# Kernel optimization log

Hardware: AMD Instinct MI355X
Metric: run time of the kernel (lower is better)

The kernel has to match this reference:

```python
import jax, jax.numpy as jnp
import numpy as np
import math

B, S, D, H = 2, 2048, 1024, 16
DH = D // H


def setup_inputs() -> dict:
    key = jax.random.key(0)
    ks = jax.random.split(key, 10)
    scale = 1.0 / math.sqrt(D)
    inp = {
        "x": jax.random.normal(ks[0], (B, S, D), dtype=jnp.float32),
        "valid_nums": jax.random.randint(ks[1], (B,), 1, S + 1, dtype=jnp.int32),
        "Wq": jax.random.normal(ks[2], (D, D), dtype=jnp.float32) * scale,
        "bq": jnp.zeros((D,), dtype=jnp.float32),
        "Wk": jax.random.normal(ks[3], (D, D), dtype=jnp.float32) * scale,
        "bk": jnp.zeros((D,), dtype=jnp.float32),
        "Wv": jax.random.normal(ks[4], (D, D), dtype=jnp.float32) * scale,
        "bv": jnp.zeros((D,), dtype=jnp.float32),
        "Wo": jax.random.normal(ks[5], (D, D), dtype=jnp.float32) * scale,
        "bo": jnp.zeros((D,), dtype=jnp.float32),
    }
    return inp


def _split_heads(t):
    # (B, S, D) -> (B, H, S, DH)
    return t.reshape(B, S, H, DH).transpose(0, 2, 1, 3)


def reference(x, valid_nums, Wq, bq, Wk, bk, Wv, bv, Wo, bo):
    q = _split_heads(x @ Wq + bq)
    k = _split_heads(x @ Wk + bk)
    v = _split_heads(x @ Wv + bv)
    scores = jnp.einsum("bhqd,bhkd->bhqk", q, k) / math.sqrt(DH)  # (B,H,S,S)
    # length mask over keys: key j valid iff j < valid_nums[b]
    key_mask = jnp.arange(S)[None, :] < valid_nums[:, None]        # (B,S)
    scores = jnp.where(key_mask[:, None, None, :], scores, -jnp.inf)
    attn = jax.nn.softmax(scores, axis=-1)
    out = jnp.einsum("bhqk,bhkd->bhqd", attn, v)                   # (B,H,S,DH)
    out = out.transpose(0, 2, 1, 3).reshape(B, S, D)
    return out @ Wo + bo
```

## Files before the change

kernel.cpp:

```cpp
#include <hip/hip_runtime.h>
#include <hip/hip_bf16.h>
#include <math.h>

static constexpr int Bb = 2, Ss = 2048, Dd = 1024, Hh = 16, DHh = 64;
static constexpr int Mm = Bb * Ss;
static constexpr int Kk = Dd;

typedef __attribute__((ext_vector_type(8))) short bf16x8;
typedef __attribute__((ext_vector_type(4))) float f32x4;
typedef unsigned short us;

__device__ inline short f2b(float f) {
    __hip_bfloat16 h = __float2bfloat16(f);
    return *reinterpret_cast<short*>(&h);
}
__device__ inline float b2f(us u) {
    __hip_bfloat16 h = *reinterpret_cast<__hip_bfloat16*>(&u);
    return __bfloat162float(h);
}
__device__ inline unsigned pk2(float lo, float hi) {
    return ((unsigned)(us)f2b(hi) << 16) | (unsigned)(us)f2b(lo);
}

__device__ inline void gload16(us* lds, const us* g) {
    __builtin_amdgcn_global_load_lds(
        (const __attribute__((address_space(1))) void*)g,
        (__attribute__((address_space(3))) void*)lds,
        16, 0, 0);
}

__global__ __launch_bounds__(256)
void xconv_kernel(const float* __restrict__ x, us* __restrict__ xb)
{
    const size_t i = ((size_t)blockIdx.x * 256 + threadIdx.x) * 8;
    float4 a = *(const float4*)(x + i);
    float4 b = *(const float4*)(x + i + 4);
    bf16x8 t;
    t[0] = f2b(a.x); t[1] = f2b(a.y); t[2] = f2b(a.z); t[3] = f2b(a.w);
    t[4] = f2b(b.x); t[5] = f2b(b.y); t[6] = f2b(b.z); t[7] = f2b(b.w);
    *(bf16x8*)(xb + i) = t;
}

__global__ __launch_bounds__(256)
void wtrans_kernel(const float* __restrict__ W, us* __restrict__ Wth,
                   us* __restrict__ Wtl, int split)
{
    __shared__ float T[64][65];
    const int n0 = blockIdx.x * 64, k0 = blockIdx.y * 64;
    const int tid = threadIdx.x;
    const int r = tid >> 2, c0 = (tid & 3) * 16;
#pragma unroll
    for (int j = 0; j < 4; ++j) {
        float4 v = *(const float4*)(W + (size_t)(k0 + r) * Dd + n0 + c0 + 4 * j);
        T[r][c0 + 4 * j + 0] = v.x;
        T[r][c0 + 4 * j + 1] = v.y;
        T[r][c0 + 4 * j + 2] = v.z;
        T[r][c0 + 4 * j + 3] = v.w;
    }
    __syncthreads();
    us hi[16], lo[16];
#pragma unroll
    for (int j = 0; j < 16; ++j) {
        float v = T[c0 + j][r];
        us h = (us)f2b(v);
        hi[j] = h;
        if (split) lo[j] = (us)f2b(v - b2f(h));
    }
    *(bf16x8*)&Wth[(size_t)(n0 + r) * Kk + k0 + c0]     = *(bf16x8*)&hi[0];
    *(bf16x8*)&Wth[(size_t)(n0 + r) * Kk + k0 + c0 + 8] = *(bf16x8*)&hi[8];
    if (split) {
        *(bf16x8*)&Wtl[(size_t)(n0 + r) * Kk + k0 + c0]     = *(bf16x8*)&lo[0];
        *(bf16x8*)&Wtl[(size_t)(n0 + r) * Kk + k0 + c0 + 8] = *(bf16x8*)&lo[8];
    }
}

__global__ __launch_bounds__(256)
void gemm_qkv_kernel(const us* __restrict__ xb, const us* __restrict__ Wt,
                     const float* __restrict__ bq, const float* __restrict__ bk,
                     const float* __restrict__ bv, us* __restrict__ QKV)
{
    __shared__ us As[128 * 64];
    __shared__ us Bs[128 * 64];
    const int tid = threadIdx.x;
    const int wave = tid >> 6, lane = tid & 63;
    const int wr = wave >> 1, wc = wave & 1;
    const int lg = lane >> 4, ll = lane & 15;
    const int col0 = blockIdx.x * 128;
    const int row0 = blockIdx.y * 128;

    f32x4 acc[4][4];
#pragma unroll
    for (int mt = 0; mt < 4; ++mt)
#pragma unroll
        for (int nt = 0; nt < 4; ++nt)
#pragma unroll
            for (int r = 0; r < 4; ++r) acc[mt][nt][r] = 0.f;

    const us* Ag = xb + (size_t)(row0 + wave * 32 + (lane >> 3)) * Kk + (lane & 7) * 8;
    const us* Bg = Wt + (size_t)(col0 + wave * 32 + (lane >> 3)) * Kk + (lane & 7) * 8;
    us* Ad = &As[(wave * 4) * 512];
    us* Bd = &Bs[(wave * 4) * 512];

    for (int k0 = 0; k0 < Kk; k0 += 64) {
        __syncthreads();
#pragma unroll
        for (int i = 0; i < 4; ++i) {
            gload16(Ad + i * 512, Ag + (size_t)(i * 8) * Kk + k0);
            gload16(Bd + i * 512, Bg + (size_t)(i * 8) * Kk + k0);
        }
        __syncthreads();
#pragma unroll
        for (int ks = 0; ks < 2; ++ks) {
            bf16x8 af[4], bfr[4];
#pragma unroll
            for (int mt = 0; mt < 4; ++mt)
                af[mt] = *(const bf16x8*)&As[(wr * 64 + mt * 16 + ll) * 64 + ks * 32 + lg * 8];
#pragma unroll
            for (int nt = 0; nt < 4; ++nt)
                bfr[nt] = *(const bf16x8*)&Bs[(wc * 64 + nt * 16 + ll) * 64 + ks * 32 + lg * 8];
#pragma unroll
            for (int mt = 0; mt < 4; ++mt)
#pragma unroll
                for (int nt = 0; nt < 4; ++nt)
                    acc[mt][nt] = __builtin_amdgcn_mfma_f32_16x16x32_bf16(af[mt], bfr[nt], acc[mt][nt], 0, 0, 0);
        }
    }

    const int z = col0 >> 10;
    const int c0 = col0 & 1023;
    const float* bias = (z == 0) ? bq : (z == 1) ? bk : bv;
    us* outz = QKV + (size_t)z * Mm * Dd;

    if (z == 2) {
#pragma unroll
        for (int mt = 0; mt < 4; ++mt)
#pragma unroll
            for (int nt = 0; nt < 4; ++nt) {
                int row = row0 + wr * 64 + mt * 16 + lg * 4;
                int col = c0 + wc * 64 + nt * 16 + ll;
                int b_ = row >> 11, s_ = row & 2047;
                float bv_ = bias[col];
                union { us u[4]; uint2 d2; } pk;
#pragma unroll
                for (int r = 0; r < 4; ++r) pk.u[r] = (us)f2b(acc[mt][nt][r] + bv_);
                *(uint2*)&outz[((size_t)(b_ * Hh * DHh) + col) * Ss + s_] = pk.d2;
            }
    } else {
#pragma unroll
        for (int mt = 0; mt < 4; ++mt)
#pragma unroll
            for (int nt = 0; nt < 4; ++nt)
#pragma unroll
                for (int r = 0; r < 4; ++r) {
                    int row = row0 + wr * 64 + mt * 16 + lg * 4 + r;
                    int col = c0 + wc * 64 + nt * 16 + ll;
                    float v = acc[mt][nt][r] + bias[col];
                    int b_ = row >> 11, s_ = row & 2047, h_ = col >> 6, d_ = col & 63;
                    outz[(((size_t)(b_ * Hh + h_)) * Ss + s_) * DHh + d_] = (us)f2b(v);
                }
    }
}

__global__ __launch_bounds__(256)
void gemm_final_kernel(const us* __restrict__ Oh, const us* __restrict__ Ol,
                       const us* __restrict__ Wth, const us* __restrict__ Wtl,
                       const float* __restrict__ bo, float* __restrict__ out)
{
    __shared__ us AhS[128 * 64];
    __shared__ us AlS[128 * 64];
    __shared__ us BhS[64 * 64];
    __shared__ us BlS[64 * 64];
    const int tid = threadIdx.x;
    const int wave = tid >> 6, lane = tid & 63;
    const int wr = wave >> 1, wc = wave & 1;
    const int lg = lane >> 4, ll = lane & 15;
    const int col0 = blockIdx.x * 64;
    const int row0 = blockIdx.y * 128;

    f32x4 acc[4][2];
#pragma unroll
    for (int mt = 0; mt < 4; ++mt)
#pragma unroll
        for (int nt = 0; nt < 2; ++nt)
#pragma unroll
            for (int r = 0; r < 4; ++r) acc[mt][nt][r] = 0.f;

    const size_t aoff = (size_t)(row0 + wave * 32 + (lane >> 3)) * Kk + (lane & 7) * 8;
    const size_t boff = (size_t)(col0 + wave * 16 + (lane >> 3)) * Kk + (lane & 7) * 8;
    const us* Ahg = Oh + aoff;
    const us* Alg = Ol + aoff;
    const us* Bhg = Wth + boff;
    const us* Blg = Wtl + boff;
    us* AhD = &AhS[(wave * 4) * 512];
    us* AlD = &AlS[(wave * 4) * 512];
    us* BhD = &BhS[(wave * 2) * 512];
    us* BlD = &BlS[(wave * 2) * 512];

    for (int k0 = 0; k0 < Kk; k0 += 64) {
        __syncthreads();
#pragma unroll
        for (int i = 0; i < 4; ++i) {
            gload16(AhD + i * 512, Ahg + (size_t)(i * 8) * Kk + k0);
            gload16(AlD + i * 512, Alg + (size_t)(i * 8) * Kk + k0);
        }
#pragma unroll
        for (int j = 0; j < 2; ++j) {
            gload16(BhD + j * 512, Bhg + (size_t)(j * 8) * Kk + k0);
            gload16(BlD + j * 512, Blg + (size_t)(j * 8) * Kk + k0);
        }
        __syncthreads();
#pragma unroll
        for (int ks = 0; ks < 2; ++ks) {
            bf16x8 ah[4], al[4], bh[2], bl[2];
#pragma unroll
            for (int mt = 0; mt < 4; ++mt) {
                ah[mt] = *(const bf16x8*)&AhS[(wr * 64 + mt * 16 + ll) * 64 + ks * 32 + lg * 8];
                al[mt] = *(const bf16x8*)&AlS[(wr * 64 + mt * 16 + ll) * 64 + ks * 32 + lg * 8];
            }
#pragma unroll
            for (int nt = 0; nt < 2; ++nt) {
                bh[nt] = *(const bf16x8*)&BhS[(wc * 32 + nt * 16 + ll) * 64 + ks * 32 + lg * 8];
                bl[nt] = *(const bf16x8*)&BlS[(wc * 32 + nt * 16 + ll) * 64 + ks * 32 + lg * 8];
            }
#pragma unroll
            for (int mt = 0; mt < 4; ++mt)
#pragma unroll
                for (int nt = 0; nt < 2; ++nt) {
                    acc[mt][nt] = __builtin_amdgcn_mfma_f32_16x16x32_bf16(ah[mt], bh[nt], acc[mt][nt], 0, 0, 0);
                    acc[mt][nt] = __builtin_amdgcn_mfma_f32_16x16x32_bf16(al[mt], bh[nt], acc[mt][nt], 0, 0, 0);
                    acc[mt][nt] = __builtin_amdgcn_mfma_f32_16x16x32_bf16(ah[mt], bl[nt], acc[mt][nt], 0, 0, 0);
                }
        }
    }

#pragma unroll
    for (int mt = 0; mt < 4; ++mt)
#pragma unroll
        for (int nt = 0; nt < 2; ++nt)
#pragma unroll
            for (int r = 0; r < 4; ++r) {
                int row = row0 + wr * 64 + mt * 16 + lg * 4 + r;
                int col = col0 + wc * 32 + nt * 16 + ll;
                out[(size_t)row * Dd + col] = acc[mt][nt][r] + bo[col];
            }
}

__global__ __launch_bounds__(256)
void attn_mfma_kernel(const us* __restrict__ Q, const us* __restrict__ K,
                      const us* __restrict__ Vt_g, const int* __restrict__ valid_nums,
                      us* __restrict__ Oh, us* __restrict__ Ol)
{
    const int bh = blockIdx.y;
    const int b  = bh >> 4, h = bh & 15;
    const int q0 = blockIdx.x * 64;
    const int tid  = threadIdx.x;
    const int wave = tid >> 6;
    const int lane = tid & 63;
    const int lg = lane >> 4;
    const int ll = lane & 15;

    const int nv = valid_nums[b];
    const int ntiles = (nv + 63) >> 6;

    const us* Qb = Q    + (size_t)bh * Ss * DHh;
    const us* Kb = K    + (size_t)bh * Ss * DHh;
    const us* Vb = Vt_g + (size_t)bh * DHh * Ss;

    __shared__ us Ks[64][68];
    __shared__ us Vs[64][68];

    bf16x8 qa[2];
    {
        const us* qrow = Qb + (size_t)(q0 + wave * 16 + ll) * DHh;
        qa[0] = *(const bf16x8*)(qrow + lg * 8);
        qa[1] = *(const bf16x8*)(qrow + 32 + lg * 8);
    }

    f32x4 o[4];
#pragma unroll
    for (int nt = 0; nt < 4; ++nt) { o[nt][0]=0.f; o[nt][1]=0.f; o[nt][2]=0.f; o[nt][3]=0.f; }
    float mq = -INFINITY, lq = 0.f;

    const int srow = tid >> 2;
    const int scol = (tid & 3) * 16;
    const float sc = 0.125f;

    for (int kt = 0; kt < ntiles; ++kt) {
        const int k0 = kt * 64;
        __syncthreads();
        {
            const us* Kr = Kb + (size_t)(k0 + srow) * DHh + scol;
            *(bf16x8*)&Ks[srow][scol]     = *(const bf16x8*)Kr;
            *(bf16x8*)&Ks[srow][scol + 8] = *(const bf16x8*)(Kr + 8);
            const us* Vr = Vb + (size_t)srow * Ss + k0 + scol;
            *(bf16x8*)&Vs[srow][scol]     = *(const bf16x8*)Vr;
            *(bf16x8*)&Vs[srow][scol + 8] = *(const bf16x8*)(Vr + 8);
        }
        __syncthreads();

        f32x4 s[4];
#pragma unroll
        for (int nt = 0; nt < 4; ++nt) { s[nt][0]=0.f; s[nt][1]=0.f; s[nt][2]=0.f; s[nt][3]=0.f; }
#pragma unroll
        for (int ks = 0; ks < 2; ++ks) {
#pragma unroll
            for (int nt = 0; nt < 4; ++nt) {
                bf16x8 kf = *(const bf16x8*)&Ks[nt * 16 + ll][ks * 32 + lg * 8];
                s[nt] = __builtin_amdgcn_mfma_f32_16x16x32_bf16(kf, qa[ks], s[nt], 0, 0, 0);
            }
        }

        float p[4][4];
        float mx = -INFINITY;
#pragma unroll
        for (int nt = 0; nt < 4; ++nt)
#pragma unroll
            for (int r = 0; r < 4; ++r) {
                int key = k0 + nt * 16 + lg * 4 + r;
                float v = (key < nv) ? s[nt][r] * sc : -INFINITY;
                p[nt][r] = v;
                mx = fmaxf(mx, v);
            }
        mx = fmaxf(mx, __shfl_xor(mx, 16));
        mx = fmaxf(mx, __shfl_xor(mx, 32));
        float mn = fmaxf(mq, mx);
        float corr = __expf(mq - mn);
        mq = mn;
        float ps = 0.f;
#pragma unroll
        for (int nt = 0; nt < 4; ++nt)
#pragma unroll
            for (int r = 0; r < 4; ++r) {
                float pv = __expf(p[nt][r] - mn);
                p[nt][r] = pv;
                ps += pv;
            }
        ps += __shfl_xor(ps, 16);
        ps += __shfl_xor(ps, 32);
        lq = lq * corr + ps;

        unsigned dw[4][2];
#pragma unroll
        for (int nt = 0; nt < 4; ++nt) {
            dw[nt][0] = pk2(p[nt][0], p[nt][1]);
            dw[nt][1] = pk2(p[nt][2], p[nt][3]);
        }

        float corr4[4];
#pragma unroll
        for (int r = 0; r < 4; ++r) corr4[r] = __shfl(corr, lg * 16 + lg * 4 + r);
#pragma unroll
        for (int nt = 0; nt < 4; ++nt)
#pragma unroll
            for (int r = 0; r < 4; ++r) o[nt][r] *= corr4[r];

        const int sA = ((2 * lg) & 3) * 16 + ll;
        const int sB = ((2 * lg + 1) & 3) * 16 + ll;
        const bool hi = (lg & 2);
#pragma unroll
        for (int ks = 0; ks < 2; ++ks) {
            unsigned a0 = (unsigned)__shfl((int)dw[2 * ks][0],     sA);
            unsigned a1 = (unsigned)__shfl((int)dw[2 * ks][1],     sA);
            unsigned a2 = (unsigned)__shfl((int)dw[2 * ks][0],     sB);
            unsigned a3 = (unsigned)__shfl((int)dw[2 * ks][1],     sB);
            unsigned b0 = (unsigned)__shfl((int)dw[2 * ks + 1][0], sA);
            unsigned b1 = (unsigned)__shfl((int)dw[2 * ks + 1][1], sA);
            unsigned b2 = (unsigned)__shfl((int)dw[2 * ks + 1][0], sB);
            unsigned b3 = (unsigned)__shfl((int)dw[2 * ks + 1][1], sB);
            union { unsigned w[4]; bf16x8 v; } pa;
            pa.w[0] = hi ? b0 : a0;
            pa.w[1] = hi ? b1 : a1;
            pa.w[2] = hi ? b2 : a2;
            pa.w[3] = hi ? b3 : a3;
#pragma unroll
            for (int nt = 0; nt < 4; ++nt) {
                bf16x8 vb = *(const bf16x8*)&Vs[nt * 16 + ll][ks * 32 + lg * 8];
                o[nt] = __builtin_amdgcn_mfma_f32_16x16x32_bf16(pa.v, vb, o[nt], 0, 0, 0);
            }
        }
    }

    float linv[4];
#pragma unroll
    for (int r = 0; r < 4; ++r) linv[r] = 1.f / __shfl(lq, lg * 16 + lg * 4 + r);
#pragma unroll
    for (int r = 0; r < 4; ++r) {
        int row = q0 + wave * 16 + lg * 4 + r;
#pragma unroll
        for (int nt = 0; nt < 4; ++nt) {
            float val = o[nt][r] * linv[r];
            us uh = (us)f2b(val);
            float rem = val - b2f(uh);
            size_t base = ((size_t)b * Ss + row) * Dd + h * DHh + nt * 16 + ll;
            Oh[base] = uh;
            Ol[base] = (us)f2b(rem);
        }
    }
}

extern "C" void kernel_launch(void* const* d_in, const int* in_sizes, int n_in,
                              void* d_out, int out_size, void* d_ws, size_t ws_size,
                              hipStream_t stream) {
    const float* x     = (const float*)d_in[0];
    const int*   valid = (const int*)d_in[1];
    const float* Wq = (const float*)d_in[2];
    const float* bq = (const float*)d_in[3];
    const float* Wk = (const float*)d_in[4];
    const float* bk = (const float*)d_in[5];
    const float* Wv = (const float*)d_in[6];
    const float* bv = (const float*)d_in[7];
    const float* Wo = (const float*)d_in[8];
    const float* bo = (const float*)d_in[9];

    const size_t per = (size_t)Mm * Dd;
    const size_t wsz = (size_t)Dd * Kk;
    us* wsp  = (us*)d_ws;
    us* QKV  = wsp;
    us* Wt   = QKV + 3 * per;
    us* OhB  = Wt + 3 * wsz;
    us* OlB  = OhB + per;
    us* Woth = OlB + per;
    us* Wotl = Woth + wsz;
    us* xb   = Wotl + wsz;

    xconv_kernel<<<(Mm * Kk) / (256 * 8), 256, 0, stream>>>(x, xb);

    dim3 tg(Dd / 64, Kk / 64);
    wtrans_kernel<<<tg, 256, 0, stream>>>(Wq, Wt + 0 * wsz, nullptr, 0);
    wtrans_kernel<<<tg, 256, 0, stream>>>(Wk, Wt + 1 * wsz, nullptr, 0);
    wtrans_kernel<<<tg, 256, 0, stream>>>(Wv, Wt + 2 * wsz, nullptr, 0);
    wtrans_kernel<<<tg, 256, 0, stream>>>(Wo, Woth, Wotl, 1);

    gemm_qkv_kernel<<<dim3(3 * Dd / 128, Mm / 128), 256, 0, stream>>>(
        xb, Wt, bq, bk, bv, QKV);

    attn_mfma_kernel<<<dim3(Ss / 64, Bb * Hh), 256, 0, stream>>>(
        QKV, QKV + per, QKV + 2 * per, valid, OhB, OlB);

    gemm_final_kernel<<<dim3(Dd / 64, Mm / 128), 256, 0, stream>>>(
        OhB, OlB, Woth, Wotl, bo, (float*)d_out);
}
```

Baseline: 166.1 us.

## Fold softmax scale into Q, lazy rescale, MFMA row sums, merge weight transposes

Folds the 1/sqrt(DH) scale into the Q projection epilogue and skips key masking on full tiles. The online-softmax rescale now runs only when some row max grows by more than a threshold. Row sums come from an extra MFMA against a ones vector instead of shuffle reductions, so probabilities are summed after bf16 rounding. The four weight-transpose launches become one 3D-grid launch, which removes launch overhead at the cost of some per-block branching.

Measured after the change: 155.1 us. -6.6%, faster.

```diff
diff --git a/kernel.cpp b/kernel.cpp
--- a/kernel.cpp
+++ b/kernel.cpp
@@ -42,10 +42,17 @@
 }
 
 __global__ __launch_bounds__(256)
-void wtrans_kernel(const float* __restrict__ W, us* __restrict__ Wth,
-                   us* __restrict__ Wtl, int split)
+void wtrans_kernel(const float* __restrict__ Wq, const float* __restrict__ Wk,
+                   const float* __restrict__ Wv, const float* __restrict__ Wo,
+                   us* __restrict__ Wt, us* __restrict__ Woth, us* __restrict__ Wotl)
 {
     __shared__ float T[64][65];
+    const int z = blockIdx.z;
+    const float* W = (z == 0) ? Wq : (z == 1) ? Wk : (z == 2) ? Wv : Wo;
+    const int split = (z == 3);
+    us* dh = split ? Woth : (Wt + (size_t)z * Dd * Kk);
+    us* dl = Wotl;
+
     const int n0 = blockIdx.x * 64, k0 = blockIdx.y * 64;
     const int tid = threadIdx.x;
     const int r = tid >> 2, c0 = (tid & 3) * 16;
@@ -66,11 +73,11 @@
         hi[j] = h;
         if (split) lo[j] = (us)f2b(v - b2f(h));
     }
-    *(bf16x8*)&Wth[(size_t)(n0 + r) * Kk + k0 + c0]     = *(bf16x8*)&hi[0];
-    *(bf16x8*)&Wth[(size_t)(n0 + r) * Kk + k0 + c0 + 8] = *(bf16x8*)&hi[8];
+    *(bf16x8*)&dh[(size_t)(n0 + r) * Kk + k0 + c0]     = *(bf16x8*)&hi[0];
+    *(bf16x8*)&dh[(size_t)(n0 + r) * Kk + k0 + c0 + 8] = *(bf16x8*)&hi[8];
     if (split) {
-        *(bf16x8*)&Wtl[(size_t)(n0 + r) * Kk + k0 + c0]     = *(bf16x8*)&lo[0];
-        *(bf16x8*)&Wtl[(size_t)(n0 + r) * Kk + k0 + c0 + 8] = *(bf16x8*)&lo[8];
+        *(bf16x8*)&dl[(size_t)(n0 + r) * Kk + k0 + c0]     = *(bf16x8*)&lo[0];
+        *(bf16x8*)&dl[(size_t)(n0 + r) * Kk + k0 + c0 + 8] = *(bf16x8*)&lo[8];
     }
 }
 
@@ -129,6 +136,7 @@
     const int z = col0 >> 10;
     const int c0 = col0 & 1023;
     const float* bias = (z == 0) ? bq : (z == 1) ? bk : bv;
+    const float osc = (z == 0) ? 0.125f : 1.0f;
     us* outz = QKV + (size_t)z * Mm * Dd;
 
     if (z == 2) {
@@ -154,7 +162,7 @@
                 for (int r = 0; r < 4; ++r) {
                     int row = row0 + wr * 64 + mt * 16 + lg * 4 + r;
                     int col = c0 + wc * 64 + nt * 16 + ll;
-                    float v = acc[mt][nt][r] + bias[col];
+                    float v = (acc[mt][nt][r] + bias[col]) * osc;
                     int b_ = row >> 11, s_ = row & 2047, h_ = col >> 6, d_ = col & 63;
                     outz[(((size_t)(b_ * Hh + h_)) * Ss + s_) * DHh + d_] = (us)f2b(v);
                 }
@@ -276,14 +284,19 @@
         qa[1] = *(const bf16x8*)(qrow + 32 + lg * 8);
     }
 
-    f32x4 o[4];
+    union { unsigned w[4]; bf16x8 v; } ones_u;
+#pragma unroll
+    for (int i = 0; i < 4; ++i) ones_u.w[i] = 0x3F803F80u;
+    const bf16x8 vones = ones_u.v;
+
+    f32x4 o[4], o4;
 #pragma unroll
     for (int nt = 0; nt < 4; ++nt) { o[nt][0]=0.f; o[nt][1]=0.f; o[nt][2]=0.f; o[nt][3]=0.f; }
-    float mq = -INFINITY, lq = 0.f;
+    o4[0]=0.f; o4[1]=0.f; o4[2]=0.f; o4[3]=0.f;
+    float mq = -INFINITY;
 
     const int srow = tid >> 2;
     const int scol = (tid & 3) * 16;
-    const float sc = 0.125f;
 
     for (int kt = 0; kt < ntiles; ++kt) {
         const int k0 = kt * 64;
@@ -311,33 +324,52 @@
         }
 
         float p[4][4];
-        float mx = -INFINITY;
-#pragma unroll
-        for (int nt = 0; nt < 4; ++nt)
-#pragma unroll
-            for (int r = 0; r < 4; ++r) {
-                int key = k0 + nt * 16 + lg * 4 + r;
-                float v = (key < nv) ? s[nt][r] * sc : -INFINITY;
-                p[nt][r] = v;
-                mx = fmaxf(mx, v);
-            }
+        float mx;
+        if (k0 + 64 <= nv) {
+#pragma unroll
+            for (int nt = 0; nt < 4; ++nt)
+#pragma unroll
+                for (int r = 0; r < 4; ++r) p[nt][r] = s[nt][r];
+            mx = fmaxf(fmaxf(fmaxf(p[0][0], p[0][1]), fmaxf(p[0][2], p[0][3])),
+                       fmaxf(fmaxf(p[1][0], p[1][1]), fmaxf(p[1][2], p[1][3])));
+            mx = fmaxf(mx,
+                 fmaxf(fmaxf(fmaxf(p[2][0], p[2][1]), fmaxf(p[2][2], p[2][3])),
+                       fmaxf(fmaxf(p[3][0], p[3][1]), fmaxf(p[3][2], p[3][3]))));
+        } else {
+            mx = -INFINITY;
+#pragma unroll
+            for (int nt = 0; nt < 4; ++nt)
+#pragma unroll
+                for (int r = 0; r < 4; ++r) {
+                    int key = k0 + nt * 16 + lg * 4 + r;
+                    float v = (key < nv) ? s[nt][r] : -INFINITY;
+                    p[nt][r] = v;
+                    mx = fmaxf(mx, v);
+                }
+        }
         mx = fmaxf(mx, __shfl_xor(mx, 16));
         mx = fmaxf(mx, __shfl_xor(mx, 32));
-        float mn = fmaxf(mq, mx);
-        float corr = __expf(mq - mn);
-        mq = mn;
-        float ps = 0.f;
+
+        const bool rescale = !__all(mx <= mq + 8.f);
+        if (rescale) {
+            float mn = fmaxf(mq, mx);
+            float corr = __expf(mq - mn);
+            mq = mn;
+            float corr4[4];
+#pragma unroll
+            for (int r = 0; r < 4; ++r) corr4[r] = __shfl(corr, lg * 16 + lg * 4 + r);
+#pragma unroll
+            for (int nt = 0; nt < 4; ++nt)
+#pragma unroll
+                for (int r = 0; r < 4; ++r) o[nt][r] *= corr4[r];
+#pragma unroll
+            for (int r = 0; r < 4; ++r) o4[r] *= corr4[r];
+        }
+
 #pragma unroll
         for (int nt = 0; nt < 4; ++nt)
 #pragma unroll
-            for (int r = 0; r < 4; ++r) {
-                float pv = __expf(p[nt][r] - mn);
-                p[nt][r] = pv;
-                ps += pv;
-            }
-        ps += __shfl_xor(ps, 16);
-        ps += __shfl_xor(ps, 32);
-        lq = lq * corr + ps;
+            for (int r = 0; r < 4; ++r) p[nt][r] = __expf(p[nt][r] - mq);
 
         unsigned dw[4][2];
 #pragma unroll
@@ -345,14 +377,6 @@
             dw[nt][0] = pk2(p[nt][0], p[nt][1]);
             dw[nt][1] = pk2(p[nt][2], p[nt][3]);
         }
-
-        float corr4[4];
-#pragma unroll
-        for (int r = 0; r < 4; ++r) corr4[r] = __shfl(corr, lg * 16 + lg * 4 + r);
-#pragma unroll
-        for (int nt = 0; nt < 4; ++nt)
-#pragma unroll
-            for (int r = 0; r < 4; ++r) o[nt][r] *= corr4[r];
 
         const int sA = ((2 * lg) & 3) * 16 + ll;
         const int sB = ((2 * lg + 1) & 3) * 16 + ll;
@@ -377,18 +401,17 @@
                 bf16x8 vb = *(const bf16x8*)&Vs[nt * 16 + ll][ks * 32 + lg * 8];
                 o[nt] = __builtin_amdgcn_mfma_f32_16x16x32_bf16(pa.v, vb, o[nt], 0, 0, 0);
             }
-        }
-    }
-
-    float linv[4];
-#pragma unroll
-    for (int r = 0; r < 4; ++r) linv[r] = 1.f / __shfl(lq, lg * 16 + lg * 4 + r);
+            o4 = __builtin_amdgcn_mfma_f32_16x16x32_bf16(pa.v, vones, o4, 0, 0, 0);
+        }
+    }
+
 #pragma unroll
     for (int r = 0; r < 4; ++r) {
         int row = q0 + wave * 16 + lg * 4 + r;
+        float linv = 1.f / o4[r];
 #pragma unroll
         for (int nt = 0; nt < 4; ++nt) {
-            float val = o[nt][r] * linv[r];
+            float val = o[nt][r] * linv;
             us uh = (us)f2b(val);
             float rem = val - b2f(uh);
             size_t base = ((size_t)b * Ss + row) * Dd + h * DHh + nt * 16 + ll;
@@ -425,11 +448,8 @@
 
     xconv_kernel<<<(Mm * Kk) / (256 * 8), 256, 0, stream>>>(x, xb);
 
-    dim3 tg(Dd / 64, Kk / 64);
-    wtrans_kernel<<<tg, 256, 0, stream>>>(Wq, Wt + 0 * wsz, nullptr, 0);
-    wtrans_kernel<<<tg, 256, 0, stream>>>(Wk, Wt + 1 * wsz, nullptr, 0);
-    wtrans_kernel<<<tg, 256, 0, stream>>>(Wv, Wt + 2 * wsz, nullptr, 0);
-    wtrans_kernel<<<tg, 256, 0, stream>>>(Wo, Woth, Wotl, 1);
+    wtrans_kernel<<<dim3(Dd / 64, Kk / 64, 4), 256, 0, stream>>>(
+        Wq, Wk, Wv, Wo, Wt, Woth, Wotl);
 
     gemm_qkv_kernel<<<dim3(3 * Dd / 128, Mm / 128), 256, 0, stream>>>(
         xb, Wt, bq, bk, bv, QKV);
```
